# Kernel tuning notes

Hardware: AMD Instinct MI355X
Metric: run time of the kernel (lower is better)

The kernel has to match this reference:

```python
import jax, jax.numpy as jnp
import numpy as np


def setup_inputs() -> dict:
    key = jax.random.key(0)
    kx, kw = jax.random.split(key)
    B, IN, OUT = 8192, 1024, 4096
    x = jax.random.normal(kx, (B, IN), dtype=jnp.float32)
    # torch.rand -> uniform [0,1)
    weight = jax.random.uniform(kw, (IN, OUT), dtype=jnp.float32)
    return {"x": x, "weight": weight}


def reference(x, weight):
    # Faithful to: (x.unsqueeze(-1) - weight).pow(2).sum(-2)
    # i.e. out[b, o] = sum_i (x[b, i] - weight[i, o])**2
    # Computed via the squared-distance expansion to avoid the
    # (B, in, out) broadcast intermediate:
    x_sq = jnp.sum(x * x, axis=-1, keepdims=True)          # (B, 1)
    w_sq = jnp.sum(weight * weight, axis=0)                # (OUT,)
    cross = jnp.matmul(x, weight)                          # (B, OUT)
    return x_sq - 2.0 * cross + w_sq
```

## Files before the change

### kernel.cpp

```cpp
#include <hip/hip_runtime.h>
#include <cstdint>
#include <cstddef>

#define B_DIM   8192
#define IN_DIM  1024
#define OUT_DIM 4096
#define KT      (IN_DIM / 16)

typedef __attribute__((ext_vector_type(8)))  short s16x8;
typedef __attribute__((ext_vector_type(16))) float f32x16;

__device__ __forceinline__ unsigned short f32_to_bf16(float f) {
    unsigned int u = __float_as_uint(f);
    u += 0x7FFFu + ((u >> 16) & 1u);
    return (unsigned short)(u >> 16);
}

__device__ __forceinline__ void async_copy16(const void* gptr, void* ldsptr) {
    __builtin_amdgcn_global_load_lds(
        (__attribute__((address_space(1))) void*)gptr,
        (__attribute__((address_space(3))) void*)ldsptr,
        16, 0, 0);
}


__global__ __launch_bounds__(256) void tile_x_kernel(
    const float* __restrict__ x, unsigned short* __restrict__ At,
    float* __restrict__ xsq, float* __restrict__ wsq)
{
    const int t  = threadIdx.x;
    const int w  = t >> 6;
    const int l  = t & 63;
    const int mt = blockIdx.x;
    const int m  = mt * 32 + (l & 31);
    const int h  = l >> 5;

    float s = 0.0f;
    #pragma unroll
    for (int c = 0; c < 16; ++c) {
        const int kt = c * 4 + w;
        const float* src = x + (size_t)m * IN_DIM + kt * 16 + h * 8;
        float4 v0 = ((const float4*)src)[0];
        float4 v1 = ((const float4*)src)[1];
        s16x8 p;
        p[0] = (short)f32_to_bf16(v0.x); p[1] = (short)f32_to_bf16(v0.y);
        p[2] = (short)f32_to_bf16(v0.z); p[3] = (short)f32_to_bf16(v0.w);
        p[4] = (short)f32_to_bf16(v1.x); p[5] = (short)f32_to_bf16(v1.y);
        p[6] = (short)f32_to_bf16(v1.z); p[7] = (short)f32_to_bf16(v1.w);
        *(s16x8*)(At + ((size_t)mt * KT + kt) * 512 + l * 8) = p;
        s += v0.x*v0.x + v0.y*v0.y + v0.z*v0.z + v0.w*v0.w
           + v1.x*v1.x + v1.y*v1.y + v1.z*v1.z + v1.w*v1.w;
    }
    s += __shfl_down(s, 32, 64);
    __shared__ float red[4][32];
    if (l < 32) red[w][l] = s;
    __syncthreads();
    if (t < 32) xsq[mt * 32 + t] = red[0][t] + red[1][t] + red[2][t] + red[3][t];

    if (blockIdx.x < OUT_DIM / 256) wsq[blockIdx.x * 256 + t] = 0.0f;
}

__global__ __launch_bounds__(256) void tile_w_kernel(
    const float* __restrict__ wgt, unsigned short* __restrict__ Bt,
    float* __restrict__ wsq)
{
    __shared__ float tile[64 * 33];
    const int t  = threadIdx.x;
    const int w  = t >> 6;
    const int l  = t & 63;
    const int nt = blockIdx.x;
    const int hf = blockIdx.y;
    const int n0 = nt * 32;
    const int rr = t >> 3;
    const int cc = t & 7;

    float s = 0.0f;
    for (int c2 = 0; c2 < 8; ++c2) {
        const int c  = hf * 8 + c2;
        const int k0 = c * 64;
        __syncthreads();
        #pragma unroll
        for (int rep = 0; rep < 2; ++rep) {
            const int r = rr + rep * 32;
            float4 v = *(const float4*)(wgt + (size_t)(k0 + r) * OUT_DIM + n0 + cc * 4);
            float* d = &tile[r * 33 + cc * 4];
            d[0] = v.x; d[1] = v.y; d[2] = v.z; d[3] = v.w;
        }
        __syncthreads();
        const int kt = c * 4 + w;
        const int n  = l & 31;
        const int kb = w * 16 + (l >> 5) * 8;
        s16x8 p;
        #pragma unroll
        for (int j = 0; j < 8; ++j) {
            float f = tile[(kb + j) * 33 + n];
            s += f * f;
            p[j] = (short)f32_to_bf16(f);
        }
        *(s16x8*)(Bt + ((size_t)nt * KT + kt) * 512 + l * 8) = p;
    }
    s += __shfl_down(s, 32, 64);
    __shared__ float red[4][32];
    if (l < 32) red[w][l] = s;
    __syncthreads();
    if (t < 32) atomicAdd(&wsq[n0 + t], red[0][t] + red[1][t] + red[2][t] + red[3][t]);
}

__global__ __launch_bounds__(256) void rbf_gemm_kernel(
    const unsigned short* __restrict__ At,
    const unsigned short* __restrict__ Bt,
    const float* __restrict__ xsq,
    const float* __restrict__ wsq,
    float* __restrict__ out)
{
    __shared__ __align__(16) unsigned short sm[2][32 * 512];

    const int t    = threadIdx.x;
    const int w    = t >> 6;
    const int l    = t & 63;
    const int l32  = l & 31;
    const int half = l >> 5;
    const int bm = blockIdx.x;
    const int bn = blockIdx.y;
    const int waveRow = w >> 1;
    const int waveCol = w & 1;

    f32x16 acc[2][2];
    #pragma unroll
    for (int mi = 0; mi < 2; ++mi)
        #pragma unroll
        for (int ni = 0; ni < 2; ++ni)
            #pragma unroll
            for (int r = 0; r < 16; ++r)
                acc[mi][ni][r] = 0.0f;

    auto stage = [&](int buf, int kti) {
        unsigned short* As = sm[buf];
        unsigned short* Bs = sm[buf] + 16 * 512;
        #pragma unroll
        for (int it = 0; it < 4; ++it) {
            async_copy16(At + ((size_t)(bm * 4 + it) * KT + kti * 4 + w) * 512 + l * 8,
                         As + (it * 4 + w) * 512);
            async_copy16(Bt + ((size_t)(bn * 4 + it) * KT + kti * 4 + w) * 512 + l * 8,
                         Bs + (it * 4 + w) * 512);
        }
    };

    stage(0, 0);
    __syncthreads();

    for (int kti = 0; kti < 16; ++kti) {
        if (kti < 15) stage((kti + 1) & 1, kti + 1);

        const unsigned short* As = sm[kti & 1];
        const unsigned short* Bs = sm[kti & 1] + 16 * 512;
        #pragma unroll
        for (int ks = 0; ks < 4; ++ks) {
            s16x8 af[2], bf[2];
            #pragma unroll
            for (int mi = 0; mi < 2; ++mi)
                af[mi] = *(const s16x8*)(As + ((waveRow * 2 + mi) * 4 + ks) * 512 + l * 8);
            #pragma unroll
            for (int ni = 0; ni < 2; ++ni)
                bf[ni] = *(const s16x8*)(Bs + ((waveCol * 2 + ni) * 4 + ks) * 512 + l * 8);
            #pragma unroll
            for (int mi = 0; mi < 2; ++mi)
                #pragma unroll
                for (int ni = 0; ni < 2; ++ni)
                    acc[mi][ni] = __builtin_amdgcn_mfma_f32_32x32x16_bf16(
                        af[mi], bf[ni], acc[mi][ni], 0, 0, 0);
        }
        __syncthreads();
    }

    #pragma unroll
    for (int mi = 0; mi < 2; ++mi) {
        const int mbase = bm * 128 + waveRow * 64 + mi * 32 + 4 * half;
        #pragma unroll
        for (int r2 = 0; r2 < 4; ++r2) {
            #pragma unroll
            for (int r1 = 0; r1 < 4; ++r1) {
                const int m  = mbase + r1 + 8 * r2;
                const float xs = xsq[m];
                #pragma unroll
                for (int ni = 0; ni < 2; ++ni) {
                    const int n = bn * 128 + waveCol * 64 + ni * 32 + l32;
                    out[(size_t)m * OUT_DIM + n] =
                        xs + wsq[n] - 2.0f * acc[mi][ni][r2 * 4 + r1];
                }
            }
        }
    }
}

extern "C" void kernel_launch(void* const* d_in, const int* in_sizes, int n_in,
                              void* d_out, int out_size, void* d_ws, size_t ws_size,
                              hipStream_t stream)
{
    const float* x   = (const float*)d_in[0];
    const float* wgt = (const float*)d_in[1];
    float* out = (float*)d_out;
    char*  ws  = (char*)d_ws;

    unsigned short* At = (unsigned short*)ws;
    unsigned short* Bt = (unsigned short*)(ws + (size_t)B_DIM * IN_DIM * 2);
    float* xsq = (float*)(ws + (size_t)B_DIM * IN_DIM * 2 + (size_t)OUT_DIM * IN_DIM * 2);
    float* wsq = xsq + B_DIM;

    tile_x_kernel<<<B_DIM / 32, 256, 0, stream>>>(x, At, xsq, wsq);
    tile_w_kernel<<<dim3(OUT_DIM / 32, 2), 256, 0, stream>>>(wgt, Bt, wsq);
    rbf_gemm_kernel<<<dim3(B_DIM / 128, OUT_DIM / 128), 256, 0, stream>>>(At, Bt, xsq, wsq, out);
}
```

Baseline: 235.3 us.

## Switch GEMM operands from bf16 to fp8 with scaled 32x32x64 MFMA

Converts x and W to fp8 (e4m3) during pre-tiling instead of bf16, repacks the panels into 64-wide K chunks, and uses the MX-scaled f8f6f4 MFMA with unit scales. This halves operand bytes in the workspace and in LDS staging, and doubles the K covered per MFMA, cutting both memory traffic and matrix-instruction count. The cost is a large precision drop in the cross term, and error in ||x||^2 - 2xW + ||W||^2 may exceed tolerance through cancellation.

After: 201.7 us. 14.3% less time.

```diff
diff --git a/kernel.cpp b/kernel.cpp
--- a/kernel.cpp
+++ b/kernel.cpp
@@ -5,16 +5,11 @@
 #define B_DIM   8192
 #define IN_DIM  1024
 #define OUT_DIM 4096
-#define KT      (IN_DIM / 16)
-
-typedef __attribute__((ext_vector_type(8)))  short s16x8;
+#define KT2     (IN_DIM / 64)
+
+typedef __attribute__((ext_vector_type(8)))  int   i32x8;
+typedef __attribute__((ext_vector_type(4)))  int   i32x4;
 typedef __attribute__((ext_vector_type(16))) float f32x16;
-
-__device__ __forceinline__ unsigned short f32_to_bf16(float f) {
-    unsigned int u = __float_as_uint(f);
-    u += 0x7FFFu + ((u >> 16) & 1u);
-    return (unsigned short)(u >> 16);
-}
 
 __device__ __forceinline__ void async_copy16(const void* gptr, void* ldsptr) {
     __builtin_amdgcn_global_load_lds(
@@ -23,33 +18,44 @@
         16, 0, 0);
 }
 
+__device__ __forceinline__ int pack4_fp8(float a, float b, float c, float d) {
+    int pk = __builtin_amdgcn_cvt_pk_fp8_f32(a, b, 0, false);
+    pk = __builtin_amdgcn_cvt_pk_fp8_f32(c, d, pk, true);
+    return pk;
+}
+
 
 __global__ __launch_bounds__(256) void tile_x_kernel(
-    const float* __restrict__ x, unsigned short* __restrict__ At,
+    const float* __restrict__ x, unsigned char* __restrict__ At,
     float* __restrict__ xsq, float* __restrict__ wsq)
 {
-    const int t  = threadIdx.x;
-    const int w  = t >> 6;
-    const int l  = t & 63;
+    const int t = threadIdx.x;
+    const int w = t >> 6;
+    const int l = t & 63;
     const int mt = blockIdx.x;
     const int m  = mt * 32 + (l & 31);
-    const int h  = l >> 5;
 
     float s = 0.0f;
     #pragma unroll
-    for (int c = 0; c < 16; ++c) {
-        const int kt = c * 4 + w;
-        const float* src = x + (size_t)m * IN_DIM + kt * 16 + h * 8;
-        float4 v0 = ((const float4*)src)[0];
-        float4 v1 = ((const float4*)src)[1];
-        s16x8 p;
-        p[0] = (short)f32_to_bf16(v0.x); p[1] = (short)f32_to_bf16(v0.y);
-        p[2] = (short)f32_to_bf16(v0.z); p[3] = (short)f32_to_bf16(v0.w);
-        p[4] = (short)f32_to_bf16(v1.x); p[5] = (short)f32_to_bf16(v1.y);
-        p[6] = (short)f32_to_bf16(v1.z); p[7] = (short)f32_to_bf16(v1.w);
-        *(s16x8*)(At + ((size_t)mt * KT + kt) * 512 + l * 8) = p;
-        s += v0.x*v0.x + v0.y*v0.y + v0.z*v0.z + v0.w*v0.w
-           + v1.x*v1.x + v1.y*v1.y + v1.z*v1.z + v1.w*v1.w;
+    for (int c = 0; c < 4; ++c) {
+        const int kt2 = c * 4 + w;
+        const float* src = x + (size_t)m * IN_DIM + kt2 * 64 + (l >> 5) * 32;
+        i32x4 lo, hi;
+        #pragma unroll
+        for (int j = 0; j < 4; ++j) {
+            float4 v = ((const float4*)src)[j];
+            s += v.x*v.x + v.y*v.y + v.z*v.z + v.w*v.w;
+            lo[j] = pack4_fp8(v.x, v.y, v.z, v.w);
+        }
+        #pragma unroll
+        for (int j = 0; j < 4; ++j) {
+            float4 v = ((const float4*)src)[4 + j];
+            s += v.x*v.x + v.y*v.y + v.z*v.z + v.w*v.w;
+            hi[j] = pack4_fp8(v.x, v.y, v.z, v.w);
+        }
+        unsigned char* pan = At + ((size_t)mt * KT2 + kt2) * 2048;
+        *(i32x4*)(pan + l * 16)        = lo;
+        *(i32x4*)(pan + 1024 + l * 16) = hi;
     }
     s += __shfl_down(s, 32, 64);
     __shared__ float red[4][32];
@@ -61,44 +67,59 @@
 }
 
 __global__ __launch_bounds__(256) void tile_w_kernel(
-    const float* __restrict__ wgt, unsigned short* __restrict__ Bt,
+    const float* __restrict__ wgt, unsigned char* __restrict__ Bt,
     float* __restrict__ wsq)
 {
-    __shared__ float tile[64 * 33];
+    __shared__ float tile[256 * 33];
     const int t  = threadIdx.x;
     const int w  = t >> 6;
     const int l  = t & 63;
     const int nt = blockIdx.x;
-    const int hf = blockIdx.y;
+    const int q  = blockIdx.y;
     const int n0 = nt * 32;
-    const int rr = t >> 3;
-    const int cc = t & 7;
-
+
+    {
+        const int rbase = t >> 2, cg = (t & 3) * 8;
+        #pragma unroll
+        for (int rep = 0; rep < 4; ++rep) {
+            const int r = rbase + rep * 64;
+            const float* src = wgt + (size_t)(q * 256 + r) * OUT_DIM + n0 + cg;
+            float4 v0 = ((const float4*)src)[0];
+            float4 v1 = ((const float4*)src)[1];
+            float* d = &tile[r * 33 + cg];
+            d[0] = v0.x; d[1] = v0.y; d[2] = v0.z; d[3] = v0.w;
+            d[4] = v1.x; d[5] = v1.y; d[6] = v1.z; d[7] = v1.w;
+        }
+    }
+    __syncthreads();
+
+    const int kt2 = q * 4 + w;
+    const int n   = l & 31;
+    const int kb  = w * 64 + (l >> 5) * 32;
     float s = 0.0f;
-    for (int c2 = 0; c2 < 8; ++c2) {
-        const int c  = hf * 8 + c2;
-        const int k0 = c * 64;
-        __syncthreads();
-        #pragma unroll
-        for (int rep = 0; rep < 2; ++rep) {
-            const int r = rr + rep * 32;
-            float4 v = *(const float4*)(wgt + (size_t)(k0 + r) * OUT_DIM + n0 + cc * 4);
-            float* d = &tile[r * 33 + cc * 4];
-            d[0] = v.x; d[1] = v.y; d[2] = v.z; d[3] = v.w;
-        }
-        __syncthreads();
-        const int kt = c * 4 + w;
-        const int n  = l & 31;
-        const int kb = w * 16 + (l >> 5) * 8;
-        s16x8 p;
-        #pragma unroll
-        for (int j = 0; j < 8; ++j) {
-            float f = tile[(kb + j) * 33 + n];
-            s += f * f;
-            p[j] = (short)f32_to_bf16(f);
-        }
-        *(s16x8*)(Bt + ((size_t)nt * KT + kt) * 512 + l * 8) = p;
-    }
+    i32x4 lo, hi;
+    #pragma unroll
+    for (int j4 = 0; j4 < 4; ++j4) {
+        float f0 = tile[(kb + j4 * 4 + 0) * 33 + n];
+        float f1 = tile[(kb + j4 * 4 + 1) * 33 + n];
+        float f2 = tile[(kb + j4 * 4 + 2) * 33 + n];
+        float f3 = tile[(kb + j4 * 4 + 3) * 33 + n];
+        s += f0*f0 + f1*f1 + f2*f2 + f3*f3;
+        lo[j4] = pack4_fp8(f0, f1, f2, f3);
+    }
+    #pragma unroll
+    for (int j4 = 0; j4 < 4; ++j4) {
+        float f0 = tile[(kb + 16 + j4 * 4 + 0) * 33 + n];
+        float f1 = tile[(kb + 16 + j4 * 4 + 1) * 33 + n];
+        float f2 = tile[(kb + 16 + j4 * 4 + 2) * 33 + n];
+        float f3 = tile[(kb + 16 + j4 * 4 + 3) * 33 + n];
+        s += f0*f0 + f1*f1 + f2*f2 + f3*f3;
+        hi[j4] = pack4_fp8(f0, f1, f2, f3);
+    }
+    unsigned char* pan = Bt + ((size_t)nt * KT2 + kt2) * 2048;
+    *(i32x4*)(pan + l * 16)        = lo;
+    *(i32x4*)(pan + 1024 + l * 16) = hi;
+
     s += __shfl_down(s, 32, 64);
     __shared__ float red[4][32];
     if (l < 32) red[w][l] = s;
@@ -107,13 +128,13 @@
 }
 
 __global__ __launch_bounds__(256) void rbf_gemm_kernel(
-    const unsigned short* __restrict__ At,
-    const unsigned short* __restrict__ Bt,
+    const unsigned char* __restrict__ At,
+    const unsigned char* __restrict__ Bt,
     const float* __restrict__ xsq,
     const float* __restrict__ wsq,
     float* __restrict__ out)
 {
-    __shared__ __align__(16) unsigned short sm[2][32 * 512];
+    __shared__ __align__(16) unsigned char sm[2][32768];
 
     const int t    = threadIdx.x;
     const int w    = t >> 6;
@@ -135,40 +156,56 @@
                 acc[mi][ni][r] = 0.0f;
 
     auto stage = [&](int buf, int kti) {
-        unsigned short* As = sm[buf];
-        unsigned short* Bs = sm[buf] + 16 * 512;
-        #pragma unroll
-        for (int it = 0; it < 4; ++it) {
-            async_copy16(At + ((size_t)(bm * 4 + it) * KT + kti * 4 + w) * 512 + l * 8,
-                         As + (it * 4 + w) * 512);
-            async_copy16(Bt + ((size_t)(bn * 4 + it) * KT + kti * 4 + w) * 512 + l * 8,
-                         Bs + (it * 4 + w) * 512);
+        unsigned char* As = sm[buf];
+        unsigned char* Bs = sm[buf] + 16384;
+        #pragma unroll
+        for (int pp = 0; pp < 2; ++pp) {
+            const int p = w * 2 + pp;
+            const unsigned char* ga = At + ((size_t)(bm * 4 + w) * KT2 + kti * 2 + pp) * 2048;
+            const unsigned char* gb = Bt + ((size_t)(bn * 4 + w) * KT2 + kti * 2 + pp) * 2048;
+            #pragma unroll
+            for (int h = 0; h < 2; ++h) {
+                async_copy16(ga + h * 1024 + l * 16, As + p * 2048 + h * 1024);
+                async_copy16(gb + h * 1024 + l * 16, Bs + p * 2048 + h * 1024);
+            }
         }
     };
 
+    auto ldfrag = [&](const unsigned char* base, int p) -> i32x8 {
+        i32x4 lo = *(const i32x4*)(base + p * 2048 + l * 16);
+        i32x4 hi = *(const i32x4*)(base + p * 2048 + 1024 + l * 16);
+        i32x8 r;
+        r[0] = lo[0]; r[1] = lo[1]; r[2] = lo[2]; r[3] = lo[3];
+        r[4] = hi[0]; r[5] = hi[1]; r[6] = hi[2]; r[7] = hi[3];
+        return r;
+    };
+
     stage(0, 0);
     __syncthreads();
 
-    for (int kti = 0; kti < 16; ++kti) {
-        if (kti < 15) stage((kti + 1) & 1, kti + 1);
-
-        const unsigned short* As = sm[kti & 1];
-        const unsigned short* Bs = sm[kti & 1] + 16 * 512;
-        #pragma unroll
-        for (int ks = 0; ks < 4; ++ks) {
-            s16x8 af[2], bf[2];
+    for (int kti = 0; kti < 8; ++kti) {
+        if (kti < 7) stage((kti + 1) & 1, kti + 1);
+
+        const unsigned char* As = sm[kti & 1];
+        const unsigned char* Bs = sm[kti & 1] + 16384;
+        #pragma unroll
+        for (int ks = 0; ks < 2; ++ks) {
+            i32x8 af[2], bf[2];
             #pragma unroll
             for (int mi = 0; mi < 2; ++mi)
-                af[mi] = *(const s16x8*)(As + ((waveRow * 2 + mi) * 4 + ks) * 512 + l * 8);
+                af[mi] = ldfrag(As, (waveRow * 2 + mi) * 2 + ks);
             #pragma unroll
             for (int ni = 0; ni < 2; ++ni)
-                bf[ni] = *(const s16x8*)(Bs + ((waveCol * 2 + ni) * 4 + ks) * 512 + l * 8);
+                bf[ni] = ldfrag(Bs, (waveCol * 2 + ni) * 2 + ks);
             #pragma unroll
             for (int mi = 0; mi < 2; ++mi)
                 #pragma unroll
                 for (int ni = 0; ni < 2; ++ni)
-                    acc[mi][ni] = __builtin_amdgcn_mfma_f32_32x32x16_bf16(
-                        af[mi], bf[ni], acc[mi][ni], 0, 0, 0);
+                    acc[mi][ni] = __builtin_amdgcn_mfma_scale_f32_32x32x64_f8f6f4(
+                        af[mi], bf[ni], acc[mi][ni],
+                        0, 0,
+                        0, 0x7F7F7F7F,
+                        0, 0x7F7F7F7F);
         }
         __syncthreads();
     }
@@ -202,12 +239,12 @@
     float* out = (float*)d_out;
     char*  ws  = (char*)d_ws;
 
-    unsigned short* At = (unsigned short*)ws;
-    unsigned short* Bt = (unsigned short*)(ws + (size_t)B_DIM * IN_DIM * 2);
-    float* xsq = (float*)(ws + (size_t)B_DIM * IN_DIM * 2 + (size_t)OUT_DIM * IN_DIM * 2);
+    unsigned char* At = (unsigned char*)ws;
+    unsigned char* Bt = (unsigned char*)(ws + (size_t)B_DIM * IN_DIM);
+    float* xsq = (float*)(ws + (size_t)B_DIM * IN_DIM + (size_t)OUT_DIM * IN_DIM);
     float* wsq = xsq + B_DIM;
 
     tile_x_kernel<<<B_DIM / 32, 256, 0, stream>>>(x, At, xsq, wsq);
-    tile_w_kernel<<<dim3(OUT_DIM / 32, 2), 256, 0, stream>>>(wgt, Bt, wsq);
+    tile_w_kernel<<<dim3(OUT_DIM / 32, 4), 256, 0, stream>>>(wgt, Bt, wsq);
     rbf_gemm_kernel<<<dim3(B_DIM / 128, OUT_DIM / 128), 256, 0, stream>>>(At, Bt, xsq, wsq, out);
 }
```
